# Optimization experiments

Measured on AMD Instinct MI355X. Metric: run time of the kernel, lower is better.

Reference implementation:

```python
import jax, jax.numpy as jnp
import numpy as np

B = 1 << 21          # shading points per batch
U_RES, CH = 400, 8   # spatial plane
A_RES, ACH = 50, 50 and 8  # placeholder, real consts below
A_RES, ACH = 50, 8   # angular planes (h/d)
HID = 32
IN_CH = CH + 2 * ACH  # 24


def _bilerp_clamp(tex, uv):
    # Bilinear interp, both axes clamped (U-plane). tex: (H,W,C), uv: (B,2) in [0,1]
    H, W, _ = tex.shape
    u = jnp.clip(uv[:, 0], 0.0, 1.0) * (W - 1)
    v = jnp.clip(uv[:, 1], 0.0, 1.0) * (H - 1)
    x0 = jnp.floor(u).astype(jnp.int32)
    x1 = jnp.clip(x0 + 1, 0, W - 1)
    y0 = jnp.floor(v).astype(jnp.int32)
    y1 = jnp.clip(y0 + 1, 0, H - 1)
    ur = (u - x0.astype(u.dtype))[:, None]
    vr = (v - y0.astype(v.dtype))[:, None]
    p00 = tex[y0, x0]; p10 = tex[y0, x1]; p01 = tex[y1, x0]; p11 = tex[y1, x1]
    return ((1 - ur) * (1 - vr) * p00 + ur * (1 - vr) * p10
            + (1 - ur) * vr * p01 + ur * vr * p11)


def _bilerp_wrap_u(tex, uv):
    # Bilinear interp wrapping the u (phi) axis, clamping v (H/D planes).
    H, W, _ = tex.shape
    u = (uv[:, 0] % 1.0) * W
    v = jnp.clip(uv[:, 1], 0.0, 1.0) * (H - 1)
    x0f = jnp.floor(u)
    x0 = x0f.astype(jnp.int32) % W
    x1 = (x0 + 1) % W
    y0 = jnp.floor(v).astype(jnp.int32)
    y1 = jnp.clip(y0 + 1, 0, H - 1)
    ur = (u - x0f)[:, None]
    vr = (v - y0.astype(v.dtype))[:, None]
    p00 = tex[y0, x0]; p10 = tex[y0, x1]; p01 = tex[y1, x0]; p11 = tex[y1, x1]
    return ((1 - ur) * (1 - vr) * p00 + ur * (1 - vr) * p10
            + (1 - ur) * vr * p01 + ur * vr * p11)


def setup_inputs() -> dict:
    key = jax.random.key(0)
    ks = jax.random.split(key, 8)
    x = jax.random.uniform(ks[0], (B, 6), dtype=jnp.float32)
    u_plane = 0.01 * jax.random.normal(ks[1], (U_RES, U_RES, CH), dtype=jnp.float32)
    h_plane = 0.01 * jax.random.normal(ks[2], (A_RES, A_RES, ACH), dtype=jnp.float32)
    d_plane = 0.01 * jax.random.normal(ks[3], (A_RES, A_RES, ACH), dtype=jnp.float32)
    def lin_w(k, fout, fin):  # torch nn.Linear default init (kaiming-uniform-ish)
        lim = 1.0 / np.sqrt(fin)
        return jax.random.uniform(k, (fout, fin), jnp.float32, -lim, lim)
    W0 = lin_w(ks[4], HID, IN_CH)
    W1 = lin_w(ks[5], HID, HID)
    W2 = lin_w(ks[6], HID, HID)
    W3 = lin_w(ks[7], 3, HID)
    return {"x": x, "u_plane": u_plane, "h_plane": h_plane, "d_plane": d_plane,
            "W0": W0, "W1": W1, "W2": W2, "W3": W3}


def reference(x, u_plane, h_plane, d_plane, W0, W1, W2, W3):
    # Split and reorder: H/D planes receive (u=phi, v=theta)
    uv = x[:, 0:2]
    h_uv = jnp.stack((x[:, 3], x[:, 2]), axis=1)
    d_uv = jnp.stack((x[:, 5], x[:, 4]), axis=1)
    fU = _bilerp_clamp(u_plane, uv)       # (B, CH)
    fH = _bilerp_wrap_u(h_plane, h_uv)    # (B, ACH)
    fD = _bilerp_wrap_u(d_plane, d_uv)    # (B, ACH)
    feat = jnp.concatenate([fU, fH, fD], axis=1)  # (B, 24)
    # Quant mode 'off' -> QLinear is a plain bias-free matmul with W^T
    h = jax.nn.relu(feat @ W0.T)
    h = jax.nn.relu(h @ W1.T)
    h = jax.nn.relu(h @ W2.T)
    return h @ W3.T  # (B, 3)
```

## Files before the change

### kernel.cpp

```cpp
#include <hip/hip_runtime.h>

typedef _Float16 half4 __attribute__((ext_vector_type(4)));
typedef _Float16 half8 __attribute__((ext_vector_type(8)));
typedef float floatx4 __attribute__((ext_vector_type(4)));

#define U_RESV 400
#define A_RESV 50

#define UHALVES (U_RESV * U_RESV * 8)
#define AHALVES (A_RESV * A_RESV * 8)
#define WOFF    (UHALVES + 2 * AHALVES)
#define WTOT    3648

__device__ __forceinline__ float clamp01(float x) { return fminf(fmaxf(x, 0.0f), 1.0f); }

__device__ __forceinline__ floatx4 mfma16(half4 a, half4 b, floatx4 c) {
    return __builtin_amdgcn_mfma_f32_16x16x16f16(a, b, c, 0, 0, 0);
}
__device__ __forceinline__ half4 zero4() {
    half4 h; h[0] = h[1] = h[2] = h[3] = (_Float16)0.f; return h;
}

__device__ __forceinline__ void cvt_chunk(const float* __restrict__ src,
                                          _Float16* __restrict__ dst, int i) {
    float4 a = *(const float4*)(src + (size_t)i * 8);
    float4 b = *(const float4*)(src + (size_t)i * 8 + 4);
    half8 h;
    h[0] = (_Float16)a.x; h[1] = (_Float16)a.y; h[2] = (_Float16)a.z; h[3] = (_Float16)a.w;
    h[4] = (_Float16)b.x; h[5] = (_Float16)b.y; h[6] = (_Float16)b.z; h[7] = (_Float16)b.w;
    *(half8*)(dst + (size_t)i * 8) = h;
}

__global__ __launch_bounds__(256) void pconv_kernel(
    const float* __restrict__ u_plane, const float* __restrict__ h_plane,
    const float* __restrict__ d_plane, const float* __restrict__ W0,
    const float* __restrict__ W1, const float* __restrict__ W2,
    const float* __restrict__ W3, _Float16* __restrict__ dst) {
    const int gid = blockIdx.x * 256 + threadIdx.x;
    const int gsz = gridDim.x * 256;
    for (int i = gid; i < UHALVES / 8; i += gsz) cvt_chunk(u_plane, dst, i);
    for (int i = gid; i < AHALVES / 8; i += gsz) cvt_chunk(h_plane, dst + UHALVES, i);
    for (int i = gid; i < AHALVES / 8; i += gsz) cvt_chunk(d_plane, dst + UHALVES + AHALVES, i);
    if (blockIdx.x == 0) {
        _Float16* w = dst + WOFF;
        for (int i = threadIdx.x; i < WTOT; i += 256) {
            float v;
            if (i < 768) {
                v = W0[i];
            } else if (i < 1920) {
                int j = i - 768, r = j / 36, c = j - r * 36;
                v = (c < 32) ? W1[r * 32 + c] : 0.f;
            } else if (i < 3072) {
                int j = i - 1920, r = j / 36, c = j - r * 36;
                v = (c < 32) ? W2[r * 32 + c] : 0.f;
            } else {
                int j = i - 3072, r = j / 36, c = j - r * 36;
                v = (r < 3 && c < 32) ? W3[r * 32 + c] : 0.f;
            }
            w[i] = (_Float16)v;
        }
    }
}

__global__ __launch_bounds__(256) void wprep_kernel(
    const float* __restrict__ W0, const float* __restrict__ W1,
    const float* __restrict__ W2, const float* __restrict__ W3,
    _Float16* __restrict__ wdst) {
    for (int i = threadIdx.x; i < WTOT; i += 256) {
        float v;
        if (i < 768) {
            v = W0[i];
        } else if (i < 1920) {
            int j = i - 768, r = j / 36, c = j - r * 36;
            v = (c < 32) ? W1[r * 32 + c] : 0.f;
        } else if (i < 3072) {
            int j = i - 1920, r = j / 36, c = j - r * 36;
            v = (c < 32) ? W2[r * 32 + c] : 0.f;
        } else {
            int j = i - 3072, r = j / 36, c = j - r * 36;
            v = (r < 3 && c < 32) ? W3[r * 32 + c] : 0.f;
        }
        wdst[i] = (_Float16)v;
    }
}


template <bool F16P>
__global__ __launch_bounds__(256, 6) void tpmlp_kernel(
    const float* __restrict__ x,
    const void* __restrict__ u_tex,
    const void* __restrict__ h_tex,
    const void* __restrict__ d_tex,
    const _Float16* __restrict__ wsw,
    float* __restrict__ out) {
    const int tid  = threadIdx.x;
    const int lane = tid & 63;
    const int wv   = tid >> 6;
    const int hf   = lane & 1;
    const int pidx = wv * 32 + (lane >> 1);
    const int q    = lane >> 4;
    const int c15  = lane & 15;

    __shared__ __align__(16) _Float16 fl[128 * 28];
    __shared__ __align__(16) _Float16 wl[WTOT];

    const uint4* wsrc = (const uint4*)wsw;
    uint4 w_a = wsrc[tid];
    uint4 w_b;
    if (tid < 456 - 256) w_b = wsrc[256 + tid];

    const size_t P = (size_t)blockIdx.x * 128 + pidx;
    const float2* xp = (const float2*)(x + P * 6);
    float2 p01v = xp[0], p23v = xp[1], p45v = xp[2];

    int oU0, oU1, oU2, oU3;  float uw00, uw10, uw01, uw11;
    {
        float u = clamp01(p01v.x) * (float)(U_RESV - 1);
        float v = clamp01(p01v.y) * (float)(U_RESV - 1);
        float x0f = floorf(u), y0f = floorf(v);
        int x0 = (int)x0f, y0 = (int)y0f;
        int x1 = min(x0 + 1, U_RESV - 1), y1 = min(y0 + 1, U_RESV - 1);
        float ur = u - x0f, vr = v - y0f;
        uw00 = (1.0f - ur) * (1.0f - vr); uw10 = ur * (1.0f - vr);
        uw01 = (1.0f - ur) * vr;          uw11 = ur * vr;
        oU0 = (y0 * U_RESV + x0) * 8 + hf * 4;
        oU1 = (y0 * U_RESV + x1) * 8 + hf * 4;
        oU2 = (y1 * U_RESV + x0) * 8 + hf * 4;
        oU3 = (y1 * U_RESV + x1) * 8 + hf * 4;
    }
    int oH0, oH1, oH2, oH3;  float hw00, hw10, hw01, hw11;
    {
        float uu = p23v.y, vv = p23v.x;
        float uf = uu - floorf(uu);
        float u = uf * (float)A_RESV;
        float v = clamp01(vv) * (float)(A_RESV - 1);
        float x0f = floorf(u), y0f = floorf(v);
        int x0 = (int)x0f;
        int x1 = x0 + 1; if (x1 == A_RESV) x1 = 0;
        int y0 = (int)y0f;
        int y1 = min(y0 + 1, A_RESV - 1);
        float ur = u - x0f, vr = v - y0f;
        hw00 = (1.0f - ur) * (1.0f - vr); hw10 = ur * (1.0f - vr);
        hw01 = (1.0f - ur) * vr;          hw11 = ur * vr;
        oH0 = (y0 * A_RESV + x0) * 8 + hf * 4;
        oH1 = (y0 * A_RESV + x1) * 8 + hf * 4;
        oH2 = (y1 * A_RESV + x0) * 8 + hf * 4;
        oH3 = (y1 * A_RESV + x1) * 8 + hf * 4;
    }
    int oD0, oD1, oD2, oD3;  float dw00, dw10, dw01, dw11;
    {
        float uu = p45v.y, vv = p45v.x;
        float uf = uu - floorf(uu);
        float u = uf * (float)A_RESV;
        float v = clamp01(vv) * (float)(A_RESV - 1);
        float x0f = floorf(u), y0f = floorf(v);
        int x0 = (int)x0f;
        int x1 = x0 + 1; if (x1 == A_RESV) x1 = 0;
        int y0 = (int)y0f;
        int y1 = min(y0 + 1, A_RESV - 1);
        float ur = u - x0f, vr = v - y0f;
        dw00 = (1.0f - ur) * (1.0f - vr); dw10 = ur * (1.0f - vr);
        dw01 = (1.0f - ur) * vr;          dw11 = ur * vr;
        oD0 = (y0 * A_RESV + x0) * 8 + hf * 4;
        oD1 = (y0 * A_RESV + x1) * 8 + hf * 4;
        oD2 = (y1 * A_RESV + x0) * 8 + hf * 4;
        oD3 = (y1 * A_RESV + x1) * 8 + hf * 4;
    }

    float4 tU0, tU1, tU2, tU3, tH0, tH1, tH2, tH3, tD0, tD1, tD2, tD3;
    half4 gU0, gU1, gU2, gU3, gH0, gH1, gH2, gH3, gD0, gD1, gD2, gD3;
    if constexpr (F16P) {
        const _Float16* up = (const _Float16*)u_tex;
        const _Float16* hp = (const _Float16*)h_tex;
        const _Float16* dp = (const _Float16*)d_tex;
        gU0 = *(const half4*)(up + oU0);
        gU1 = *(const half4*)(up + oU1);
        gU2 = *(const half4*)(up + oU2);
        gU3 = *(const half4*)(up + oU3);
        gH0 = *(const half4*)(hp + oH0);
        gH1 = *(const half4*)(hp + oH1);
        gH2 = *(const half4*)(hp + oH2);
        gH3 = *(const half4*)(hp + oH3);
        gD0 = *(const half4*)(dp + oD0);
        gD1 = *(const half4*)(dp + oD1);
        gD2 = *(const half4*)(dp + oD2);
        gD3 = *(const half4*)(dp + oD3);
    } else {
        const float* up = (const float*)u_tex;
        const float* hp = (const float*)h_tex;
        const float* dp = (const float*)d_tex;
        tU0 = *(const float4*)(up + oU0);
        tU1 = *(const float4*)(up + oU1);
        tU2 = *(const float4*)(up + oU2);
        tU3 = *(const float4*)(up + oU3);
        tH0 = *(const float4*)(hp + oH0);
        tH1 = *(const float4*)(hp + oH1);
        tH2 = *(const float4*)(hp + oH2);
        tH3 = *(const float4*)(hp + oH3);
        tD0 = *(const float4*)(dp + oD0);
        tD1 = *(const float4*)(dp + oD1);
        tD2 = *(const float4*)(dp + oD2);
        tD3 = *(const float4*)(dp + oD3);
    }
    __builtin_amdgcn_sched_barrier(0);

    {
        uint4* dst = (uint4*)wl;
        dst[tid] = w_a;
        if (tid < 456 - 256) dst[256 + tid] = w_b;
    }
    asm volatile("s_waitcnt lgkmcnt(0)" ::: "memory");
    __builtin_amdgcn_s_barrier();

    float fU[4], fH[4], fD[4];
    if constexpr (F16P) {
#pragma unroll
        for (int i = 0; i < 4; ++i) {
            float r = (float)gU0[i] * uw00;
            r = fmaf((float)gU1[i], uw10, r);
            r = fmaf((float)gU2[i], uw01, r);
            r = fmaf((float)gU3[i], uw11, r);
            fU[i] = r;
        }
#pragma unroll
        for (int i = 0; i < 4; ++i) {
            float r = (float)gH0[i] * hw00;
            r = fmaf((float)gH1[i], hw10, r);
            r = fmaf((float)gH2[i], hw01, r);
            r = fmaf((float)gH3[i], hw11, r);
            fH[i] = r;
        }
#pragma unroll
        for (int i = 0; i < 4; ++i) {
            float r = (float)gD0[i] * dw00;
            r = fmaf((float)gD1[i], dw10, r);
            r = fmaf((float)gD2[i], dw01, r);
            r = fmaf((float)gD3[i], dw11, r);
            fD[i] = r;
        }
    } else {
        {
            const float* a = (const float*)&tU0; const float* b = (const float*)&tU1;
            const float* c = (const float*)&tU2; const float* d = (const float*)&tU3;
#pragma unroll
            for (int i = 0; i < 4; ++i) {
                float r = a[i] * uw00;
                r = fmaf(b[i], uw10, r);
                r = fmaf(c[i], uw01, r);
                r = fmaf(d[i], uw11, r);
                fU[i] = r;
            }
        }
        {
            const float* a = (const float*)&tH0; const float* b = (const float*)&tH1;
            const float* c = (const float*)&tH2; const float* d = (const float*)&tH3;
#pragma unroll
            for (int i = 0; i < 4; ++i) {
                float r = a[i] * hw00;
                r = fmaf(b[i], hw10, r);
                r = fmaf(c[i], hw01, r);
                r = fmaf(d[i], hw11, r);
                fH[i] = r;
            }
        }
        {
            const float* a = (const float*)&tD0; const float* b = (const float*)&tD1;
            const float* c = (const float*)&tD2; const float* d = (const float*)&tD3;
#pragma unroll
            for (int i = 0; i < 4; ++i) {
                float r = a[i] * dw00;
                r = fmaf(b[i], dw10, r);
                r = fmaf(c[i], dw01, r);
                r = fmaf(d[i], dw11, r);
                fD[i] = r;
            }
        }
    }

    {
        _Float16* row = fl + pidx * 28;
        half4 hU, hH, hD;
#pragma unroll
        for (int i = 0; i < 4; ++i) {
            hU[i] = (_Float16)fU[i];
            hH[i] = (_Float16)fH[i];
            hD[i] = (_Float16)fD[i];
        }
        *(half4*)(row + hf * 4)      = hU;
        *(half4*)(row + 8 + hf * 4)  = hH;
        *(half4*)(row + 16 + hf * 4) = hD;
    }
    asm volatile("s_waitcnt lgkmcnt(0)" ::: "memory");
    __builtin_amdgcn_sched_barrier(0);

    floatx4 zf; zf[0] = 0.f; zf[1] = 0.f; zf[2] = 0.f; zf[3] = 0.f;
    const _Float16* wb = fl + (size_t)wv * 32 * 28;
    const _Float16* w0l = wl;
    const _Float16* w1l = wl + 768;
    const _Float16* w2l = wl + 1920;
    const _Float16* w3l = wl + 3072;

    half4 b0[2], b1[2];
#pragma unroll
    for (int j = 0; j < 2; ++j) {
        const _Float16* r = wb + (size_t)(j * 16 + c15) * 28;
        b0[j] = *(const half4*)(r + q * 4);
        b1[j] = (q < 2) ? *(const half4*)(r + 16 + q * 4) : zero4();
    }

    floatx4 cc[2][2];
#pragma unroll
    for (int m = 0; m < 2; ++m) {
        half4 a0 = *(const half4*)(w0l + (size_t)(16 * m + c15) * 24 + q * 4);
        half4 a1 = (q < 2) ? *(const half4*)(w0l + (size_t)(16 * m + c15) * 24 + 16 + q * 4) : zero4();
#pragma unroll
        for (int j = 0; j < 2; ++j)
            cc[m][j] = mfma16(a1, b1[j], mfma16(a0, b0[j], zf));
    }
#pragma unroll
    for (int j = 0; j < 2; ++j)
#pragma unroll
        for (int e = 0; e < 4; ++e) {
            b0[j][e] = (_Float16)fmaxf(cc[0][j][e], 0.f);
            b1[j][e] = (_Float16)fmaxf(cc[1][j][e], 0.f);
        }

#pragma unroll
    for (int m = 0; m < 2; ++m) {
        half4 a0 = *(const half4*)(w1l + (size_t)(16 * m + c15) * 36 + q * 4);
        half4 a1 = *(const half4*)(w1l + (size_t)(16 * m + c15) * 36 + 16 + q * 4);
#pragma unroll
        for (int j = 0; j < 2; ++j)
            cc[m][j] = mfma16(a1, b1[j], mfma16(a0, b0[j], zf));
    }
#pragma unroll
    for (int j = 0; j < 2; ++j)
#pragma unroll
        for (int e = 0; e < 4; ++e) {
            b0[j][e] = (_Float16)fmaxf(cc[0][j][e], 0.f);
            b1[j][e] = (_Float16)fmaxf(cc[1][j][e], 0.f);
        }

#pragma unroll
    for (int m = 0; m < 2; ++m) {
        half4 a0 = *(const half4*)(w2l + (size_t)(16 * m + c15) * 36 + q * 4);
        half4 a1 = *(const half4*)(w2l + (size_t)(16 * m + c15) * 36 + 16 + q * 4);
#pragma unroll
        for (int j = 0; j < 2; ++j)
            cc[m][j] = mfma16(a1, b1[j], mfma16(a0, b0[j], zf));
    }
#pragma unroll
    for (int j = 0; j < 2; ++j)
#pragma unroll
        for (int e = 0; e < 4; ++e) {
            b0[j][e] = (_Float16)fmaxf(cc[0][j][e], 0.f);
            b1[j][e] = (_Float16)fmaxf(cc[1][j][e], 0.f);
        }

    floatx4 c3[2];
    {
        half4 a0 = *(const half4*)(w3l + (size_t)c15 * 36 + q * 4);
        half4 a1 = *(const half4*)(w3l + (size_t)c15 * 36 + 16 + q * 4);
#pragma unroll
        for (int j = 0; j < 2; ++j)
            c3[j] = mfma16(a1, b1[j], mfma16(a0, b0[j], zf));
    }

    if (lane < 16) {
        const size_t base = (size_t)blockIdx.x * 128 + (size_t)wv * 32;
#pragma unroll
        for (int j = 0; j < 2; ++j) {
            size_t p = base + (size_t)j * 16 + lane;
            float* o = out + p * 3;
            float3 v3 = make_float3(c3[j][0], c3[j][1], c3[j][2]);
            *(float3*)o = v3;
        }
    }
}

extern "C" void kernel_launch(void* const* d_in, const int* in_sizes, int n_in,
                              void* d_out, int out_size, void* d_ws, size_t ws_size,
                              hipStream_t stream) {
    const float* x       = (const float*)d_in[0];
    const float* u_plane = (const float*)d_in[1];
    const float* h_plane = (const float*)d_in[2];
    const float* d_plane = (const float*)d_in[3];
    const float* W0      = (const float*)d_in[4];
    const float* W1      = (const float*)d_in[5];
    const float* W2      = (const float*)d_in[6];
    const float* W3      = (const float*)d_in[7];
    float* out = (float*)d_out;
    _Float16* wsw = (_Float16*)d_ws;

    int n = in_sizes[0] / 6;
    int grid = n / 128;

    const size_t need = ((size_t)WOFF + WTOT) * 2;
    if (ws_size >= need) {
        pconv_kernel<<<648, 256, 0, stream>>>(u_plane, h_plane, d_plane,
                                              W0, W1, W2, W3, wsw);
        tpmlp_kernel<true><<<grid, 256, 0, stream>>>(
            x, (const void*)wsw, (const void*)(wsw + UHALVES),
            (const void*)(wsw + UHALVES + AHALVES), wsw + WOFF, out);
    } else {
        wprep_kernel<<<1, 256, 0, stream>>>(W0, W1, W2, W3, wsw);
        tpmlp_kernel<false><<<grid, 256, 0, stream>>>(
            x, (const void*)u_plane, (const void*)h_plane, (const void*)d_plane,
            wsw, out);
    }
}
```

Before: 77.15 us.

## Process one point per thread with 256-point blocks and padded W0 layout

Each thread now handles a whole shading point, gathering all 8 channels with half8 loads, where before two threads shared a point with half4 loads. Blocks cover 256 points, so each wave runs 4 MFMA column tiles instead of 2, and the per-block weight blob load is amortized over twice as many points. W0 rows are padded to stride 28 to reduce LDS bank conflicts, and ReLU is applied on packed half4 after conversion. The cost is more registers per thread, so launch bounds drop to 4 blocks per SM, and the LDS feature buffer doubles in size.

New measurement: 75.48 us. 1.02x faster.

```diff
diff --git a/kernel.cpp b/kernel.cpp
--- a/kernel.cpp
+++ b/kernel.cpp
@@ -10,7 +10,11 @@
 #define UHALVES (U_RESV * U_RESV * 8)
 #define AHALVES (A_RESV * A_RESV * 8)
 #define WOFF    (UHALVES + 2 * AHALVES)
-#define WTOT    3648
+#define W0OFF   0
+#define W1OFF   896
+#define W2OFF   2048
+#define W3OFF   3200
+#define WTOT    3776
 
 __device__ __forceinline__ float clamp01(float x) { return fminf(fmaxf(x, 0.0f), 1.0f); }
 
@@ -19,6 +23,16 @@
 }
 __device__ __forceinline__ half4 zero4() {
     half4 h; h[0] = h[1] = h[2] = h[3] = (_Float16)0.f; return h;
+}
+__device__ __forceinline__ half4 relu4(half4 v) {
+#if __has_builtin(__builtin_elementwise_max)
+    return __builtin_elementwise_max(v, zero4());
+#else
+    half4 r;
+#pragma unroll
+    for (int i = 0; i < 4; ++i) r[i] = v[i] > (_Float16)0.f ? v[i] : (_Float16)0.f;
+    return r;
+#endif
 }
 
 __device__ __forceinline__ void cvt_chunk(const float* __restrict__ src,
@@ -29,6 +43,30 @@
     h[0] = (_Float16)a.x; h[1] = (_Float16)a.y; h[2] = (_Float16)a.z; h[3] = (_Float16)a.w;
     h[4] = (_Float16)b.x; h[5] = (_Float16)b.y; h[6] = (_Float16)b.z; h[7] = (_Float16)b.w;
     *(half8*)(dst + (size_t)i * 8) = h;
+}
+
+__device__ __forceinline__ void wblob_fill(const float* __restrict__ W0,
+                                           const float* __restrict__ W1,
+                                           const float* __restrict__ W2,
+                                           const float* __restrict__ W3,
+                                           _Float16* __restrict__ w, int tid) {
+    for (int i = tid; i < WTOT; i += 256) {
+        float v;
+        if (i < W1OFF) {
+            int r = i / 28, c = i - r * 28;
+            v = (c < 24) ? W0[r * 24 + c] : 0.f;
+        } else if (i < W2OFF) {
+            int j = i - W1OFF, r = j / 36, c = j - r * 36;
+            v = (c < 32) ? W1[r * 32 + c] : 0.f;
+        } else if (i < W3OFF) {
+            int j = i - W2OFF, r = j / 36, c = j - r * 36;
+            v = (c < 32) ? W2[r * 32 + c] : 0.f;
+        } else {
+            int j = i - W3OFF, r = j / 36, c = j - r * 36;
+            v = (r < 3 && c < 32) ? W3[r * 32 + c] : 0.f;
+        }
+        w[i] = (_Float16)v;
+    }
 }
 
 __global__ __launch_bounds__(256) void pconv_kernel(
@@ -41,52 +79,19 @@
     for (int i = gid; i < UHALVES / 8; i += gsz) cvt_chunk(u_plane, dst, i);
     for (int i = gid; i < AHALVES / 8; i += gsz) cvt_chunk(h_plane, dst + UHALVES, i);
     for (int i = gid; i < AHALVES / 8; i += gsz) cvt_chunk(d_plane, dst + UHALVES + AHALVES, i);
-    if (blockIdx.x == 0) {
-        _Float16* w = dst + WOFF;
-        for (int i = threadIdx.x; i < WTOT; i += 256) {
-            float v;
-            if (i < 768) {
-                v = W0[i];
-            } else if (i < 1920) {
-                int j = i - 768, r = j / 36, c = j - r * 36;
-                v = (c < 32) ? W1[r * 32 + c] : 0.f;
-            } else if (i < 3072) {
-                int j = i - 1920, r = j / 36, c = j - r * 36;
-                v = (c < 32) ? W2[r * 32 + c] : 0.f;
-            } else {
-                int j = i - 3072, r = j / 36, c = j - r * 36;
-                v = (r < 3 && c < 32) ? W3[r * 32 + c] : 0.f;
-            }
-            w[i] = (_Float16)v;
-        }
-    }
+    if (blockIdx.x == 0) wblob_fill(W0, W1, W2, W3, dst + WOFF, threadIdx.x);
 }
 
 __global__ __launch_bounds__(256) void wprep_kernel(
     const float* __restrict__ W0, const float* __restrict__ W1,
     const float* __restrict__ W2, const float* __restrict__ W3,
     _Float16* __restrict__ wdst) {
-    for (int i = threadIdx.x; i < WTOT; i += 256) {
-        float v;
-        if (i < 768) {
-            v = W0[i];
-        } else if (i < 1920) {
-            int j = i - 768, r = j / 36, c = j - r * 36;
-            v = (c < 32) ? W1[r * 32 + c] : 0.f;
-        } else if (i < 3072) {
-            int j = i - 1920, r = j / 36, c = j - r * 36;
-            v = (c < 32) ? W2[r * 32 + c] : 0.f;
-        } else {
-            int j = i - 3072, r = j / 36, c = j - r * 36;
-            v = (r < 3 && c < 32) ? W3[r * 32 + c] : 0.f;
-        }
-        wdst[i] = (_Float16)v;
-    }
+    wblob_fill(W0, W1, W2, W3, wdst, threadIdx.x);
 }
 
 
 template <bool F16P>
-__global__ __launch_bounds__(256, 6) void tpmlp_kernel(
+__global__ __launch_bounds__(256, 4) void tpmlp_kernel(
     const float* __restrict__ x,
     const void* __restrict__ u_tex,
     const void* __restrict__ h_tex,
@@ -96,20 +101,18 @@
     const int tid  = threadIdx.x;
     const int lane = tid & 63;
     const int wv   = tid >> 6;
-    const int hf   = lane & 1;
-    const int pidx = wv * 32 + (lane >> 1);
     const int q    = lane >> 4;
     const int c15  = lane & 15;
 
-    __shared__ __align__(16) _Float16 fl[128 * 28];
+    __shared__ __align__(16) _Float16 fl[256 * 28];
     __shared__ __align__(16) _Float16 wl[WTOT];
 
     const uint4* wsrc = (const uint4*)wsw;
     uint4 w_a = wsrc[tid];
     uint4 w_b;
-    if (tid < 456 - 256) w_b = wsrc[256 + tid];
-
-    const size_t P = (size_t)blockIdx.x * 128 + pidx;
+    if (tid < 472 - 256) w_b = wsrc[256 + tid];
+
+    const size_t P = (size_t)blockIdx.x * 256 + tid;
     const float2* xp = (const float2*)(x + P * 6);
     float2 p01v = xp[0], p23v = xp[1], p45v = xp[2];
 
@@ -123,10 +126,10 @@
         float ur = u - x0f, vr = v - y0f;
         uw00 = (1.0f - ur) * (1.0f - vr); uw10 = ur * (1.0f - vr);
         uw01 = (1.0f - ur) * vr;          uw11 = ur * vr;
-        oU0 = (y0 * U_RESV + x0) * 8 + hf * 4;
-        oU1 = (y0 * U_RESV + x1) * 8 + hf * 4;
-        oU2 = (y1 * U_RESV + x0) * 8 + hf * 4;
-        oU3 = (y1 * U_RESV + x1) * 8 + hf * 4;
+        oU0 = (y0 * U_RESV + x0) * 8;
+        oU1 = (y0 * U_RESV + x1) * 8;
+        oU2 = (y1 * U_RESV + x0) * 8;
+        oU3 = (y1 * U_RESV + x1) * 8;
     }
     int oH0, oH1, oH2, oH3;  float hw00, hw10, hw01, hw11;
     {
@@ -142,10 +145,10 @@
         float ur = u - x0f, vr = v - y0f;
         hw00 = (1.0f - ur) * (1.0f - vr); hw10 = ur * (1.0f - vr);
         hw01 = (1.0f - ur) * vr;          hw11 = ur * vr;
-        oH0 = (y0 * A_RESV + x0) * 8 + hf * 4;
-        oH1 = (y0 * A_RESV + x1) * 8 + hf * 4;
-        oH2 = (y1 * A_RESV + x0) * 8 + hf * 4;
-        oH3 = (y1 * A_RESV + x1) * 8 + hf * 4;
+        oH0 = (y0 * A_RESV + x0) * 8;
+        oH1 = (y0 * A_RESV + x1) * 8;
+        oH2 = (y1 * A_RESV + x0) * 8;
+        oH3 = (y1 * A_RESV + x1) * 8;
     }
     int oD0, oD1, oD2, oD3;  float dw00, dw10, dw01, dw11;
     {
@@ -161,61 +164,62 @@
         float ur = u - x0f, vr = v - y0f;
         dw00 = (1.0f - ur) * (1.0f - vr); dw10 = ur * (1.0f - vr);
         dw01 = (1.0f - ur) * vr;          dw11 = ur * vr;
-        oD0 = (y0 * A_RESV + x0) * 8 + hf * 4;
-        oD1 = (y0 * A_RESV + x1) * 8 + hf * 4;
-        oD2 = (y1 * A_RESV + x0) * 8 + hf * 4;
-        oD3 = (y1 * A_RESV + x1) * 8 + hf * 4;
-    }
-
-    float4 tU0, tU1, tU2, tU3, tH0, tH1, tH2, tH3, tD0, tD1, tD2, tD3;
-    half4 gU0, gU1, gU2, gU3, gH0, gH1, gH2, gH3, gD0, gD1, gD2, gD3;
+        oD0 = (y0 * A_RESV + x0) * 8;
+        oD1 = (y0 * A_RESV + x1) * 8;
+        oD2 = (y1 * A_RESV + x0) * 8;
+        oD3 = (y1 * A_RESV + x1) * 8;
+    }
+
+    half8 gU0, gU1, gU2, gU3, gH0, gH1, gH2, gH3, gD0, gD1, gD2, gD3;
+    float4 sU0, sU1, sU2, sU3, sH0, sH1, sH2, sH3, sD0, sD1, sD2, sD3;
+    float4 rU0, rU1, rU2, rU3, rH0, rH1, rH2, rH3, rD0, rD1, rD2, rD3;
     if constexpr (F16P) {
         const _Float16* up = (const _Float16*)u_tex;
         const _Float16* hp = (const _Float16*)h_tex;
         const _Float16* dp = (const _Float16*)d_tex;
-        gU0 = *(const half4*)(up + oU0);
-        gU1 = *(const half4*)(up + oU1);
-        gU2 = *(const half4*)(up + oU2);
-        gU3 = *(const half4*)(up + oU3);
-        gH0 = *(const half4*)(hp + oH0);
-        gH1 = *(const half4*)(hp + oH1);
-        gH2 = *(const half4*)(hp + oH2);
-        gH3 = *(const half4*)(hp + oH3);
-        gD0 = *(const half4*)(dp + oD0);
-        gD1 = *(const half4*)(dp + oD1);
-        gD2 = *(const half4*)(dp + oD2);
-        gD3 = *(const half4*)(dp + oD3);
+        gU0 = *(const half8*)(up + oU0);
+        gU1 = *(const half8*)(up + oU1);
+        gU2 = *(const half8*)(up + oU2);
+        gU3 = *(const half8*)(up + oU3);
+        gH0 = *(const half8*)(hp + oH0);
+        gH1 = *(const half8*)(hp + oH1);
+        gH2 = *(const half8*)(hp + oH2);
+        gH3 = *(const half8*)(hp + oH3);
+        gD0 = *(const half8*)(dp + oD0);
+        gD1 = *(const half8*)(dp + oD1);
+        gD2 = *(const half8*)(dp + oD2);
+        gD3 = *(const half8*)(dp + oD3);
     } else {
         const float* up = (const float*)u_tex;
         const float* hp = (const float*)h_tex;
         const float* dp = (const float*)d_tex;
-        tU0 = *(const float4*)(up + oU0);
-        tU1 = *(const float4*)(up + oU1);
-        tU2 = *(const float4*)(up + oU2);
-        tU3 = *(const float4*)(up + oU3);
-        tH0 = *(const float4*)(hp + oH0);
-        tH1 = *(const float4*)(hp + oH1);
-        tH2 = *(const float4*)(hp + oH2);
-        tH3 = *(const float4*)(hp + oH3);
-        tD0 = *(const float4*)(dp + oD0);
-        tD1 = *(const float4*)(dp + oD1);
-        tD2 = *(const float4*)(dp + oD2);
-        tD3 = *(const float4*)(dp + oD3);
+        sU0 = *(const float4*)(up + oU0); rU0 = *(const float4*)(up + oU0 + 4);
+        sU1 = *(const float4*)(up + oU1); rU1 = *(const float4*)(up + oU1 + 4);
+        sU2 = *(const float4*)(up + oU2); rU2 = *(const float4*)(up + oU2 + 4);
+        sU3 = *(const float4*)(up + oU3); rU3 = *(const float4*)(up + oU3 + 4);
+        sH0 = *(const float4*)(hp + oH0); rH0 = *(const float4*)(hp + oH0 + 4);
+        sH1 = *(const float4*)(hp + oH1); rH1 = *(const float4*)(hp + oH1 + 4);
+        sH2 = *(const float4*)(hp + oH2); rH2 = *(const float4*)(hp + oH2 + 4);
+        sH3 = *(const float4*)(hp + oH3); rH3 = *(const float4*)(hp + oH3 + 4);
+        sD0 = *(const float4*)(dp + oD0); rD0 = *(const float4*)(dp + oD0 + 4);
+        sD1 = *(const float4*)(dp + oD1); rD1 = *(const float4*)(dp + oD1 + 4);
+        sD2 = *(const float4*)(dp + oD2); rD2 = *(const float4*)(dp + oD2 + 4);
+        sD3 = *(const float4*)(dp + oD3); rD3 = *(const float4*)(dp + oD3 + 4);
     }
     __builtin_amdgcn_sched_barrier(0);
 
     {
         uint4* dst = (uint4*)wl;
         dst[tid] = w_a;
-        if (tid < 456 - 256) dst[256 + tid] = w_b;
+        if (tid < 472 - 256) dst[256 + tid] = w_b;
     }
     asm volatile("s_waitcnt lgkmcnt(0)" ::: "memory");
     __builtin_amdgcn_s_barrier();
 
-    float fU[4], fH[4], fD[4];
+    float fU[8], fH[8], fD[8];
     if constexpr (F16P) {
 #pragma unroll
-        for (int i = 0; i < 4; ++i) {
+        for (int i = 0; i < 8; ++i) {
             float r = (float)gU0[i] * uw00;
             r = fmaf((float)gU1[i], uw10, r);
             r = fmaf((float)gU2[i], uw01, r);
@@ -223,7 +227,7 @@
             fU[i] = r;
         }
 #pragma unroll
-        for (int i = 0; i < 4; ++i) {
+        for (int i = 0; i < 8; ++i) {
             float r = (float)gH0[i] * hw00;
             r = fmaf((float)gH1[i], hw10, r);
             r = fmaf((float)gH2[i], hw01, r);
@@ -231,7 +235,7 @@
             fH[i] = r;
         }
 #pragma unroll
-        for (int i = 0; i < 4; ++i) {
+        for (int i = 0; i < 8; ++i) {
             float r = (float)gD0[i] * dw00;
             r = fmaf((float)gD1[i], dw10, r);
             r = fmaf((float)gD2[i], dw01, r);
@@ -239,141 +243,158 @@
             fD[i] = r;
         }
     } else {
-        {
-            const float* a = (const float*)&tU0; const float* b = (const float*)&tU1;
-            const float* c = (const float*)&tU2; const float* d = (const float*)&tU3;
-#pragma unroll
-            for (int i = 0; i < 4; ++i) {
-                float r = a[i] * uw00;
-                r = fmaf(b[i], uw10, r);
-                r = fmaf(c[i], uw01, r);
-                r = fmaf(d[i], uw11, r);
-                fU[i] = r;
-            }
-        }
-        {
-            const float* a = (const float*)&tH0; const float* b = (const float*)&tH1;
-            const float* c = (const float*)&tH2; const float* d = (const float*)&tH3;
-#pragma unroll
-            for (int i = 0; i < 4; ++i) {
-                float r = a[i] * hw00;
-                r = fmaf(b[i], hw10, r);
-                r = fmaf(c[i], hw01, r);
-                r = fmaf(d[i], hw11, r);
-                fH[i] = r;
-            }
-        }
-        {
-            const float* a = (const float*)&tD0; const float* b = (const float*)&tD1;
-            const float* c = (const float*)&tD2; const float* d = (const float*)&tD3;
-#pragma unroll
-            for (int i = 0; i < 4; ++i) {
-                float r = a[i] * dw00;
-                r = fmaf(b[i], dw10, r);
-                r = fmaf(c[i], dw01, r);
-                r = fmaf(d[i], dw11, r);
-                fD[i] = r;
-            }
-        }
-    }
-
-    {
-        _Float16* row = fl + pidx * 28;
-        half4 hU, hH, hD;
-#pragma unroll
-        for (int i = 0; i < 4; ++i) {
+        const float* a;
+        const float* b;
+        const float* c;
+        const float* d;
+#pragma unroll
+        for (int i = 0; i < 8; ++i) {
+            a = i < 4 ? (const float*)&sU0 : (const float*)&rU0;
+            b = i < 4 ? (const float*)&sU1 : (const float*)&rU1;
+            c = i < 4 ? (const float*)&sU2 : (const float*)&rU2;
+            d = i < 4 ? (const float*)&sU3 : (const float*)&rU3;
+            int k = i & 3;
+            float r = a[k] * uw00;
+            r = fmaf(b[k], uw10, r);
+            r = fmaf(c[k], uw01, r);
+            r = fmaf(d[k], uw11, r);
+            fU[i] = r;
+        }
+#pragma unroll
+        for (int i = 0; i < 8; ++i) {
+            a = i < 4 ? (const float*)&sH0 : (const float*)&rH0;
+            b = i < 4 ? (const float*)&sH1 : (const float*)&rH1;
+            c = i < 4 ? (const float*)&sH2 : (const float*)&rH2;
+            d = i < 4 ? (const float*)&sH3 : (const float*)&rH3;
+            int k = i & 3;
+            float r = a[k] * hw00;
+            r = fmaf(b[k], hw10, r);
+            r = fmaf(c[k], hw01, r);
+            r = fmaf(d[k], hw11, r);
+            fH[i] = r;
+        }
+#pragma unroll
+        for (int i = 0; i < 8; ++i) {
+            a = i < 4 ? (const float*)&sD0 : (const float*)&rD0;
+            b = i < 4 ? (const float*)&sD1 : (const float*)&rD1;
+            c = i < 4 ? (const float*)&sD2 : (const float*)&rD2;
+            d = i < 4 ? (const float*)&sD3 : (const float*)&rD3;
+            int k = i & 3;
+            float r = a[k] * dw00;
+            r = fmaf(b[k], dw10, r);
+            r = fmaf(c[k], dw01, r);
+            r = fmaf(d[k], dw11, r);
+            fD[i] = r;
+        }
+    }
+
+    {
+        _Float16* row = fl + tid * 28;
+        half8 hU, hH, hD;
+#pragma unroll
+        for (int i = 0; i < 8; ++i) {
             hU[i] = (_Float16)fU[i];
             hH[i] = (_Float16)fH[i];
             hD[i] = (_Float16)fD[i];
         }
-        *(half4*)(row + hf * 4)      = hU;
-        *(half4*)(row + 8 + hf * 4)  = hH;
-        *(half4*)(row + 16 + hf * 4) = hD;
+        *(half8*)(row)      = hU;
+        *(half8*)(row + 8)  = hH;
+        *(half8*)(row + 16) = hD;
     }
     asm volatile("s_waitcnt lgkmcnt(0)" ::: "memory");
     __builtin_amdgcn_sched_barrier(0);
 
     floatx4 zf; zf[0] = 0.f; zf[1] = 0.f; zf[2] = 0.f; zf[3] = 0.f;
-    const _Float16* wb = fl + (size_t)wv * 32 * 28;
-    const _Float16* w0l = wl;
-    const _Float16* w1l = wl + 768;
-    const _Float16* w2l = wl + 1920;
-    const _Float16* w3l = wl + 3072;
-
-    half4 b0[2], b1[2];
-#pragma unroll
-    for (int j = 0; j < 2; ++j) {
+    const _Float16* wb = fl + (size_t)wv * 64 * 28;
+    const _Float16* w0l = wl + W0OFF;
+    const _Float16* w1l = wl + W1OFF;
+    const _Float16* w2l = wl + W2OFF;
+    const _Float16* w3l = wl + W3OFF;
+
+    half4 b0[4], b1[4];
+#pragma unroll
+    for (int j = 0; j < 4; ++j) {
         const _Float16* r = wb + (size_t)(j * 16 + c15) * 28;
         b0[j] = *(const half4*)(r + q * 4);
         b1[j] = (q < 2) ? *(const half4*)(r + 16 + q * 4) : zero4();
     }
 
-    floatx4 cc[2][2];
+    floatx4 cc[2][4];
 #pragma unroll
     for (int m = 0; m < 2; ++m) {
-        half4 a0 = *(const half4*)(w0l + (size_t)(16 * m + c15) * 24 + q * 4);
-        half4 a1 = (q < 2) ? *(const half4*)(w0l + (size_t)(16 * m + c15) * 24 + 16 + q * 4) : zero4();
-#pragma unroll
-        for (int j = 0; j < 2; ++j)
+        half4 a0 = *(const half4*)(w0l + (size_t)(16 * m + c15) * 28 + q * 4);
+        half4 a1 = (q < 2) ? *(const half4*)(w0l + (size_t)(16 * m + c15) * 28 + 16 + q * 4) : zero4();
+#pragma unroll
+        for (int j = 0; j < 4; ++j)
             cc[m][j] = mfma16(a1, b1[j], mfma16(a0, b0[j], zf));
     }
 #pragma unroll
-    for (int j = 0; j < 2; ++j)
+    for (int j = 0; j < 4; ++j) {
 #pragma unroll
         for (int e = 0; e < 4; ++e) {
-            b0[j][e] = (_Float16)fmaxf(cc[0][j][e], 0.f);
-            b1[j][e] = (_Float16)fmaxf(cc[1][j][e], 0.f);
-        }
+            b0[j][e] = (_Float16)cc[0][j][e];
+            b1[j][e] = (_Float16)cc[1][j][e];
+        }
+        b0[j] = relu4(b0[j]);
+        b1[j] = relu4(b1[j]);
+    }
 
 #pragma unroll
     for (int m = 0; m < 2; ++m) {
         half4 a0 = *(const half4*)(w1l + (size_t)(16 * m + c15) * 36 + q * 4);
         half4 a1 = *(const half4*)(w1l + (size_t)(16 * m + c15) * 36 + 16 + q * 4);
 #pragma unroll
-        for (int j = 0; j < 2; ++j)
+        for (int j = 0; j < 4; ++j)
             cc[m][j] = mfma16(a1, b1[j], mfma16(a0, b0[j], zf));
     }
 #pragma unroll
-    for (int j = 0; j < 2; ++j)
+    for (int j = 0; j < 4; ++j) {
 #pragma unroll
         for (int e = 0; e < 4; ++e) {
-            b0[j][e] = (_Float16)fmaxf(cc[0][j][e], 0.f);
-            b1[j][e] = (_Float16)fmaxf(cc[1][j][e], 0.f);
-        }
+            b0[j][e] = (_Float16)cc[0][j][e];
+            b1[j][e] = (_Float16)cc[1][j][e];
+        }
+        b0[j] = relu4(b0[j]);
+        b1[j] = relu4(b1[j]);
+    }
 
 #pragma unroll
     for (int m = 0; m < 2; ++m) {
         half4 a0 = *(const half4*)(w2l + (size_t)(16 * m + c15) * 36 + q * 4);
         half4 a1 = *(const half4*)(w2l + (size_t)(16 * m + c15) * 36 + 16 + q * 4);
 #pragma unroll
-        for (int j = 0; j < 2; ++j)
+        for (int j = 0; j < 4; ++j)
             cc[m][j] = mfma16(a1, b1[j], mfma16(a0, b0[j], zf));
     }
 #pragma unroll
-    for (int j = 0; j < 2; ++j)
+    for (int j = 0; j < 4; ++j) {
 #pragma unroll
         for (int e = 0; e < 4; ++e) {
-            b0[j][e] = (_Float16)fmaxf(cc[0][j][e], 0.f);
-            b1[j][e] = (_Float16)fmaxf(cc[1][j][e], 0.f);
-        }
-
-    floatx4 c3[2];
+            b0[j][e] = (_Float16)cc[0][j][e];
+            b1[j][e] = (_Float16)cc[1][j][e];
+        }
+        b0[j] = relu4(b0[j]);
+        b1[j] = relu4(b1[j]);
+    }
+
+    floatx4 c3[4];
     {
         half4 a0 = *(const half4*)(w3l + (size_t)c15 * 36 + q * 4);
         half4 a1 = *(const half4*)(w3l + (size_t)c15 * 36 + 16 + q * 4);
 #pragma unroll
-        for (int j = 0; j < 2; ++j)
+        for (int j = 0; j < 4; ++j)
             c3[j] = mfma16(a1, b1[j], mfma16(a0, b0[j], zf));
     }
 
     if (lane < 16) {
-        const size_t base = (size_t)blockIdx.x * 128 + (size_t)wv * 32;
-#pragma unroll
-        for (int j = 0; j < 2; ++j) {
+        const size_t base = (size_t)blockIdx.x * 256 + (size_t)wv * 64;
+#pragma unroll
+        for (int j = 0; j < 4; ++j) {
             size_t p = base + (size_t)j * 16 + lane;
             float* o = out + p * 3;
-            float3 v3 = make_float3(c3[j][0], c3[j][1], c3[j][2]);
-            *(float3*)o = v3;
+            o[0] = c3[j][0];
+            o[1] = c3[j][1];
+            o[2] = c3[j][2];
         }
     }
 }
@@ -393,7 +414,7 @@
     _Float16* wsw = (_Float16*)d_ws;
 
     int n = in_sizes[0] / 6;
-    int grid = n / 128;
+    int grid = n / 256;
 
     const size_t need = ((size_t)WOFF + WTOT) * 2;
     if (ws_size >= need) {
```
